# Kernel optimization log

Measured on AMD Instinct MI355X. Metric: run time of the kernel, lower is better.

## Reference

```python
import jax, jax.numpy as jnp
import numpy as np

B, T, V, D, U = 128, 512, 50000, 256, 256


def setup_inputs() -> dict:
    key = jax.random.key(0)
    ks = jax.random.split(key, 16)

    def n(k, shape, s=0.05):
        return jax.random.normal(k, shape, dtype=jnp.float32) * s

    inp = {
        "tokens": jax.random.randint(ks[0], (B, T), 0, V, dtype=jnp.int32),
        "emb": n(ks[1], (V, D)),
    }
    dims = [D, U, U, U]
    i = 2
    for l in range(4):
        inp[f"Wx{l}"] = n(ks[i], (dims[l], 3 * U)); i += 1
        inp[f"Wh{l}"] = n(ks[i], (U, 3 * U)); i += 1
        inp[f"bx{l}"] = jnp.zeros((3 * U,), jnp.float32)
        inp[f"bh{l}"] = jnp.zeros((3 * U,), jnp.float32)
    inp["Wd1"] = n(ks[i], (U, U)); i += 1
    inp["bd1"] = jnp.zeros((U,), jnp.float32)
    inp["Wd2"] = n(ks[i], (U, 1)); i += 1
    inp["bd2"] = jnp.zeros((1,), jnp.float32)
    return inp


def _gru_layer(x_seq, Wx, Wh, bx, bh):
    # x_seq: [T, B, d_in]. Keras GRUCell math with reset_after=True.
    # Precompute all input projections in one big GEMM (efficient form).
    xp = jnp.einsum('tbd,dk->tbk', x_seq, Wx) + bx  # [T, B, 3U]
    h0 = jnp.zeros((x_seq.shape[1], Wh.shape[0]), x_seq.dtype)

    def step(h, xp_t):
        rec = h @ Wh + bh                      # recurrent proj + recurrent bias
        xz, xr, xh = jnp.split(xp_t, 3, axis=-1)
        rz, rr, rh = jnp.split(rec, 3, axis=-1)
        z = jax.nn.sigmoid(xz + rz)            # update gate
        r = jax.nn.sigmoid(xr + rr)            # reset gate
        hh = jnp.tanh(xh + r * rh)             # candidate (reset applied after rec matmul)
        hn = z * h + (1.0 - z) * hh
        return hn, hn

    _, hs = jax.lax.scan(step, h0, xp)
    return hs  # [T, B, U]


def reference(tokens, emb,
              Wx0, Wh0, bx0, bh0,
              Wx1, Wh1, bx1, bh1,
              Wx2, Wh2, bx2, bh2,
              Wx3, Wh3, bx3, bh3,
              Wd1, bd1, Wd2, bd2):
    x = emb[tokens]                    # [B, T, D] embedding lookup
    x = jnp.transpose(x, (1, 0, 2))    # [T, B, D] time-major for scan
    for Wx, Wh, bx, bh in ((Wx0, Wh0, bx0, bh0), (Wx1, Wh1, bx1, bh1),
                           (Wx2, Wh2, bx2, bh2), (Wx3, Wh3, bx3, bh3)):
        x = _gru_layer(x, Wx, Wh, bx, bh)
    out = x[-1]                        # last timestep of top layer: [B, U]
    h = jax.nn.relu(out @ Wd1 + bd1)   # Dense(units) + ReLU (dropout off at inference)
    logit = h @ Wd2 + bd2              # Dense(1)
    return jax.nn.sigmoid(logit)       # [B, 1]
```

## Files before the change

### kernel.cpp

```cpp
#include <hip/hip_runtime.h>
#include <stdint.h>


#define TT 512
#define RX 16
#define RH 64

typedef __bf16 bf16x8 __attribute__((ext_vector_type(8)));
typedef float f32x4 __attribute__((ext_vector_type(4)));
typedef int i32x4 __attribute__((ext_vector_type(4)));

#define FLAGS_BYTES (128*256)
#define XPRING_E ((size_t)RX*768*16)
#define HRING_E  ((size_t)RH*16*256)
#define WS_XP_OFF ((size_t)FLAGS_BYTES)
#define WS_H_OFF  (WS_XP_OFF + (size_t)32*XPRING_E*2)
#define WS_HF_OFF (WS_H_OFF  + (size_t)32*HRING_E*2)

struct Params {
  const int* tokens;
  const float* emb;
  const float* Wx[4];
  const float* Wh[4];
  const float* bx[4];
  const float* bh[4];
  uint8_t* ws;
};

#define SCOPE_AGENT __HIP_MEMORY_SCOPE_AGENT

__device__ __forceinline__ uint32_t* flagp(uint8_t* ws, int kind, int g, int l){
  return (uint32_t*)(ws + ((size_t)(kind*32 + g*4 + l) * 256));
}
__device__ __forceinline__ uint32_t aload(uint32_t* p){
  return __hip_atomic_load(p, __ATOMIC_RELAXED, SCOPE_AGENT);
}
__device__ __forceinline__ void astore(uint32_t* p, uint32_t v){
  __hip_atomic_store(p, v, __ATOMIC_RELAXED, SCOPE_AGENT);
}
__device__ __forceinline__ void st_coh_b64(void* p, unsigned long long v){
  asm volatile("global_store_dwordx2 %0, %1, off sc0 sc1" :: "v"(p), "v"(v) : "memory");
}
__device__ __forceinline__ void st_coh_b128(void* p, i32x4 v){
  asm volatile("global_store_dwordx4 %0, %1, off sc0 sc1" :: "v"(p), "v"(v) : "memory");
}
__device__ __forceinline__ unsigned long long ld_coh_b64(const void* p){
  unsigned long long r;
  asm volatile("global_load_dwordx2 %0, %1, off sc0 sc1" : "=v"(r) : "v"(p));
  return r;
}
__device__ __forceinline__ i32x4 ld_coh_b128(const void* p){
  i32x4 r;
  asm volatile("global_load_dwordx4 %0, %1, off sc0 sc1" : "=v"(r) : "v"(p));
  return r;
}
__device__ __forceinline__ void wait_vm0(){
  asm volatile("s_waitcnt vmcnt(0)" ::: "memory");
}
__device__ __forceinline__ unsigned short f2b(float f){
  __bf16 b = (__bf16)f; unsigned short u; __builtin_memcpy(&u, &b, 2); return u;
}
__device__ __forceinline__ float b2f(unsigned short u){
  __bf16 b; __builtin_memcpy(&b, &u, 2); return (float)b;
}
__device__ __forceinline__ f32x4 up4(unsigned long long q){
  f32x4 r;
  #pragma unroll
  for (int i=0;i<4;++i) r[i] = b2f((unsigned short)(q >> (16*i)));
  return r;
}
__device__ __forceinline__ unsigned long long pk4(f32x4 v){
  unsigned long long q = 0;
  #pragma unroll
  for (int i=0;i<4;++i) q |= ((unsigned long long)f2b(v[i])) << (16*i);
  return q;
}
__device__ __forceinline__ float sigf(float x){ return 1.f/(1.f + __expf(-x)); }
__device__ __forceinline__ float tanh_(float x){ return 2.f/(1.f + __expf(-2.f*x)) - 1.f; }

__global__ __launch_bounds__(512, 2) void gru_pipeline(Params p){
  const int bid = blockIdx.x;
  const int g = bid >> 3;
  const int s = bid & 7;
  const int l = s >> 1;
  const bool isXp = (s & 1) == 0;
  const int tid = threadIdx.x;
  const int w = tid >> 6;
  const int lane = tid & 63;
  const int lg = lane >> 4;
  const int lc = lane & 15;

  __shared__ int dead;
  __shared__ __align__(16) unsigned short h_stage[2][16*256];
  __shared__ __align__(16) unsigned short h_lds[16*256];
  if (tid == 0) dead = 0;
  int budget = 1 << 22;

  if (isXp) {
    const float* W = p.Wx[l];
    bf16x8 wx[6][8];
    #pragma unroll
    for (int nt=0; nt<6; ++nt){
      const int col = w*96 + nt*16 + lc;
      #pragma unroll
      for (int kt=0; kt<8; ++kt){
        const int k0 = kt*32 + lg*8;
        bf16x8 v;
        #pragma unroll
        for (int e=0; e<8; ++e) v[e] = (__bf16)W[(size_t)(k0+e)*768 + col];
        wx[nt][kt] = v;
      }
    }
    float bias[6];
    #pragma unroll
    for (int nt=0; nt<6; ++nt){
      const int col = w*96 + nt*16 + lc;
      bias[nt] = p.bx[l][col] + (col < 512 ? p.bh[l][col] : 0.f);
    }
    uint32_t* prodXp = flagp(p.ws, 0, g, l);
    uint32_t* prodH  = (l>0) ? flagp(p.ws, 1, g, l-1) : nullptr;
    uint32_t* consXp = flagp(p.ws, 2, g, l);
    uint32_t* consH  = (l>0) ? flagp(p.ws, 3, g, l-1) : nullptr;
    __bf16* xr = (__bf16*)(p.ws + WS_XP_OFF) + (size_t)(g*4+l)*XPRING_E;
    const __bf16* hr = (l>0) ? ((const __bf16*)(p.ws + WS_H_OFF) + (size_t)(g*4+(l-1))*HRING_E) : nullptr;
    uint32_t consSeen = 0, prodSeen = 0;
    const int sm = tid >> 5, sc = tid & 31;

    if (l > 0){
      if (tid == 0){
        while (prodSeen < 1u){
          prodSeen = aload(prodH);
          if (prodSeen < 1u){ if(--budget<0){dead=1;break;} __builtin_amdgcn_s_sleep(2); }
        }
      }
      __syncthreads();
      if (!dead){
        i32x4 v = ld_coh_b128(hr + (size_t)sm*256 + sc*8);
        wait_vm0(); __builtin_amdgcn_sched_barrier(0);
        *(i32x4*)&h_stage[0][(sm*256 + sc*8) ^ ((sm&7)<<3)] = v;
      }
    } else {
      const int tok = p.tokens[(size_t)(g*16+sm)*TT];
      const float* er = p.emb + (size_t)tok*256 + sc*8;
      const float4 u0 = *(const float4*)er;
      const float4 u1 = *(const float4*)(er+4);
      bf16x8 v;
      v[0]=(__bf16)u0.x; v[1]=(__bf16)u0.y; v[2]=(__bf16)u0.z; v[3]=(__bf16)u0.w;
      v[4]=(__bf16)u1.x; v[5]=(__bf16)u1.y; v[6]=(__bf16)u1.z; v[7]=(__bf16)u1.w;
      *(bf16x8*)&h_stage[0][(sm*256 + sc*8) ^ ((sm&7)<<3)] = v;
    }

    for (int t=0; t<TT; ++t){
      if (tid == 0){
        if (l > 0){
          const uint32_t need = (uint32_t)((t+2 < TT) ? t+2 : TT);
          while (prodSeen < need){
            prodSeen = aload(prodH);
            if (prodSeen < need){ if(--budget<0){dead=1;break;} __builtin_amdgcn_s_sleep(2); }
          }
        }
        if (t >= RX){
          const uint32_t need2 = (uint32_t)(t - RX + 1);
          while (consSeen < need2){
            consSeen = aload(consXp);
            if (consSeen < need2){ if(--budget<0){dead=1;break;} __builtin_amdgcn_s_sleep(2); }
          }
        }
      }
      __syncthreads();
      if (dead) break;
      if (tid == 0 && t > 0){
        astore(prodXp, (uint32_t)t);
        if (l > 0) astore(consH, (uint32_t)(t+1));
      }

      i32x4 stg;
      const bool haveStg = (l > 0) && (t+1 < TT);
      if (haveStg){
        stg = ld_coh_b128(hr + (size_t)((t+1)&(RH-1))*16*256 + sm*256 + sc*8);
      } else if (l == 0 && t+1 < TT){
        const int tok = p.tokens[(size_t)(g*16+sm)*TT + (t+1)];
        const float* er = p.emb + (size_t)tok*256 + sc*8;
        const float4 u0 = *(const float4*)er;
        const float4 u1 = *(const float4*)(er+4);
        bf16x8 v;
        v[0]=(__bf16)u0.x; v[1]=(__bf16)u0.y; v[2]=(__bf16)u0.z; v[3]=(__bf16)u0.w;
        v[4]=(__bf16)u1.x; v[5]=(__bf16)u1.y; v[6]=(__bf16)u1.z; v[7]=(__bf16)u1.w;
        *(bf16x8*)&h_stage[(t+1)&1][(sm*256 + sc*8) ^ ((sm&7)<<3)] = v;
      }

      const unsigned short* hsrc = h_stage[t&1];
      f32x4 acc[6];
      #pragma unroll
      for (int nt=0; nt<6; ++nt) acc[nt] = (f32x4){bias[nt],bias[nt],bias[nt],bias[nt]};
      #pragma unroll
      for (int kt=0; kt<8; ++kt){
        const bf16x8 a = *(const bf16x8*)&hsrc[(lc*256 + kt*32 + lg*8) ^ ((lc&7)<<3)];
        #pragma unroll
        for (int nt=0; nt<6; ++nt)
          acc[nt] = __builtin_amdgcn_mfma_f32_16x16x32_bf16(a, wx[nt][kt], acc[nt], 0, 0, 0);
      }
      if (haveStg){
        wait_vm0(); __builtin_amdgcn_sched_barrier(0);
        *(i32x4*)&h_stage[(t+1)&1][(sm*256 + sc*8) ^ ((sm&7)<<3)] = stg;
      }
      __bf16* dst = xr + (size_t)(t&(RX-1))*768*16;
      #pragma unroll
      for (int nt=0; nt<6; ++nt){
        const int col = w*96 + nt*16 + lc;
        st_coh_b64(dst + col*16 + lg*4, pk4(acc[nt]));
      }
    }
    wait_vm0();
    __syncthreads();
    if (tid == 0 && !dead){
      astore(prodXp, (uint32_t)TT);
      if (l > 0) astore(consH, (uint32_t)TT);
    }
  } else {
    const float* W = p.Wh[l];
    bf16x8 wh[6][8];
    #pragma unroll
    for (int nt=0; nt<6; ++nt){
      const int col = 256*(nt>>1) + w*32 + 16*(nt&1) + lc;
      #pragma unroll
      for (int kt=0; kt<8; ++kt){
        const int k0 = kt*32 + lg*8;
        bf16x8 v;
        #pragma unroll
        for (int e=0; e<8; ++e) v[e] = (__bf16)W[(size_t)(k0+e)*768 + col];
        wh[nt][kt] = v;
      }
    }
    float bhh[2];
    #pragma unroll
    for (int q=0; q<2; ++q) bhh[q] = p.bh[l][512 + w*32 + 16*q + lc];

    uint32_t* prodXp = flagp(p.ws, 0, g, l);
    uint32_t* prodH  = (l<3) ? flagp(p.ws, 1, g, l) : nullptr;
    uint32_t* consXp = flagp(p.ws, 2, g, l);
    uint32_t* consH  = (l<3) ? flagp(p.ws, 3, g, l) : nullptr;
    const __bf16* xr = (const __bf16*)(p.ws + WS_XP_OFF) + (size_t)(g*4+l)*XPRING_E;
    __bf16* hrw = (l<3) ? ((__bf16*)(p.ws + WS_H_OFF) + (size_t)(g*4+l)*HRING_E) : nullptr;
    float* hf = (float*)(p.ws + WS_HF_OFF);

    for (int i=tid; i<2048; i+=512) ((uint32_t*)h_lds)[i] = 0;
    f32x4 hprev[2] = {(f32x4){0.f,0.f,0.f,0.f},(f32x4){0.f,0.f,0.f,0.f}};
    uint32_t consSeen = 0, prodSeen = 0;

    for (int t=0; t<TT; ++t){
      if (tid == 0){
        while (prodSeen < (uint32_t)(t+1)){
          prodSeen = aload(prodXp);
          if (prodSeen < (uint32_t)(t+1)){ if(--budget<0){dead=1;break;} __builtin_amdgcn_s_sleep(2); }
        }
        if (l < 3 && t > RH){
          while (consSeen < (uint32_t)(t - RH)){
            consSeen = aload(consH);
            if (consSeen < (uint32_t)(t - RH)){ if(--budget<0){dead=1;break;} __builtin_amdgcn_s_sleep(2); }
          }
        }
      }
      __syncthreads();
      if (dead) break;

      const __bf16* xb = xr + (size_t)(t&(RX-1))*768*16;
      unsigned long long xpld[6];
      #pragma unroll
      for (int nt=0; nt<6; ++nt){
        const int col = 256*(nt>>1) + w*32 + 16*(nt&1) + lc;
        xpld[nt] = ld_coh_b64(xb + col*16 + lg*4);
      }
      if (l < 3 && t > 0){
        const i32x4 ev = *(const i32x4*)&h_lds[(lc*256 + w*32 + lg*8) ^ ((lc&7)<<3)];
        st_coh_b128(hrw + (size_t)((t-1)&(RH-1))*16*256 + lc*256 + w*32 + lg*8, ev);
      }
      f32x4 acc[6];
      #pragma unroll
      for (int nt=0; nt<6; ++nt) acc[nt] = (f32x4){0.f,0.f,0.f,0.f};
      #pragma unroll
      for (int kt=0; kt<8; ++kt){
        const bf16x8 a = *(const bf16x8*)&h_lds[(lc*256 + kt*32 + lg*8) ^ ((lc&7)<<3)];
        #pragma unroll
        for (int nt=0; nt<6; ++nt)
          acc[nt] = __builtin_amdgcn_mfma_f32_16x16x32_bf16(a, wh[nt][kt], acc[nt], 0, 0, 0);
      }
      wait_vm0(); __builtin_amdgcn_sched_barrier(0);
      #pragma unroll
      for (int q=0; q<2; ++q){
        const f32x4 xz = up4(xpld[q]);
        const f32x4 xr_ = up4(xpld[2+q]);
        const f32x4 xh = up4(xpld[4+q]);
        #pragma unroll
        for (int e=0; e<4; ++e){
          const float z = sigf(xz[e] + acc[q][e]);
          const float r = sigf(xr_[e] + acc[2+q][e]);
          const float c = tanh_(xh[e] + r*(acc[4+q][e] + bhh[q]));
          hprev[q][e] = z*hprev[q][e] + (1.f - z)*c;
        }
      }
      __syncthreads();
      #pragma unroll
      for (int q=0; q<2; ++q){
        const int j = w*32 + 16*q + lc;
        #pragma unroll
        for (int r2=0; r2<4; ++r2){
          const int m = lg*4 + r2;
          h_lds[(m*256 + j) ^ ((m&7)<<3)] = f2b(hprev[q][r2]);
        }
      }
      if (l == 3 && t == TT-1){
        #pragma unroll
        for (int q=0; q<2; ++q){
          const int j = w*32 + 16*q + lc;
          #pragma unroll
          for (int r2=0; r2<4; ++r2) hf[(size_t)(g*16 + lg*4 + r2)*256 + j] = hprev[q][r2];
        }
      }
      __syncthreads();
      if (tid == 0){
        if (l < 3 && t > 0) astore(prodH, (uint32_t)t);
        astore(consXp, (uint32_t)(t+1));
      }
    }
    if (!dead){
      if (l < 3){
        const i32x4 ev = *(const i32x4*)&h_lds[(lc*256 + w*32 + lg*8) ^ ((lc&7)<<3)];
        st_coh_b128(hrw + (size_t)((TT-1)&(RH-1))*16*256 + lc*256 + w*32 + lg*8, ev);
        wait_vm0();
        __syncthreads();
        if (tid == 0) astore(prodH, (uint32_t)TT);
      }
      if (tid == 0) astore(consXp, (uint32_t)TT);
    }
  }
}

__global__ __launch_bounds__(256) void dense_head(const float* __restrict__ hf,
    const float* __restrict__ Wd1, const float* __restrict__ bd1,
    const float* __restrict__ Wd2, const float* __restrict__ bd2,
    float* __restrict__ out){
  const int m = blockIdx.x;
  const int n = threadIdx.x;
  __shared__ float hs[256];
  __shared__ float red[256];
  hs[n] = hf[(size_t)m*256 + n];
  __syncthreads();
  float acc = bd1[n];
  #pragma unroll 8
  for (int k=0; k<256; ++k) acc = fmaf(hs[k], Wd1[(size_t)k*256 + n], acc);
  const float rl = fmaxf(acc, 0.f);
  red[n] = rl * Wd2[n];
  __syncthreads();
  for (int off=128; off>0; off>>=1){
    if (n < off) red[n] += red[n+off];
    __syncthreads();
  }
  if (n == 0) out[m] = 1.f/(1.f + __expf(-(red[0] + bd2[0])));
}

extern "C" void kernel_launch(void* const* d_in, const int* in_sizes, int n_in,
                              void* d_out, int out_size, void* d_ws, size_t ws_size,
                              hipStream_t stream){
  (void)in_sizes; (void)n_in; (void)out_size; (void)ws_size;
  Params p;
  p.tokens = (const int*)d_in[0];
  p.emb    = (const float*)d_in[1];
  for (int l=0; l<4; ++l){
    p.Wx[l] = (const float*)d_in[2+4*l];
    p.Wh[l] = (const float*)d_in[3+4*l];
    p.bx[l] = (const float*)d_in[4+4*l];
    p.bh[l] = (const float*)d_in[5+4*l];
  }
  p.ws = (uint8_t*)d_ws;
  hipMemsetAsync(d_ws, 0, FLAGS_BYTES, stream);
  gru_pipeline<<<dim3(64), dim3(512), 0, stream>>>(p);
  dense_head<<<dim3(128), dim3(256), 0, stream>>>(
      (const float*)((uint8_t*)d_ws + WS_HF_OFF),
      (const float*)d_in[18], (const float*)d_in[19],
      (const float*)d_in[20], (const float*)d_in[21],
      (float*)d_out);
}
```

Measured before the change: 2.904 ms.

## Batch cross-block flag handshakes every 4 steps and double-buffer recurrent state in LDS

Inter-block producer/consumer flag polling and publishing now happen once per chunk of CH=4 timesteps rather than every step. The recurrent blocks double-buffer the hidden state in shared memory, which removes one barrier per step. They also prefetch the next step's input projection one step ahead, using partial vmcnt waits in place of full drains. This cuts per-step global atomic traffic and barrier latency on the serial recurrence. The cost is coarser pipeline slack, which could delay downstream layers. The hand-counted vmcnt values are fragile and may break ordering.

```diff
diff --git a/kernel.cpp b/kernel.cpp
--- a/kernel.cpp
+++ b/kernel.cpp
@@ -5,6 +5,7 @@
 #define TT 512
 #define RX 16
 #define RH 64
+#define CH 4
 
 typedef __bf16 bf16x8 __attribute__((ext_vector_type(8)));
 typedef float f32x4 __attribute__((ext_vector_type(4)));
@@ -54,9 +55,9 @@
   asm volatile("global_load_dwordx4 %0, %1, off sc0 sc1" : "=v"(r) : "v"(p));
   return r;
 }
-__device__ __forceinline__ void wait_vm0(){
-  asm volatile("s_waitcnt vmcnt(0)" ::: "memory");
-}
+#define WAITVM(N) asm volatile("s_waitcnt vmcnt(" #N ")" ::: "memory")
+#define BARRIER_LGKM() asm volatile("s_waitcnt lgkmcnt(0)\n\ts_barrier" ::: "memory")
+
 __device__ __forceinline__ unsigned short f2b(float f){
   __bf16 b = (__bf16)f; unsigned short u; __builtin_memcpy(&u, &b, 2); return u;
 }
@@ -78,7 +79,7 @@
 __device__ __forceinline__ float sigf(float x){ return 1.f/(1.f + __expf(-x)); }
 __device__ __forceinline__ float tanh_(float x){ return 2.f/(1.f + __expf(-2.f*x)) - 1.f; }
 
-__global__ __launch_bounds__(512, 2) void gru_pipeline(Params p){
+__global__ __launch_bounds__(512) void gru_pipeline(Params p){
   const int bid = blockIdx.x;
   const int g = bid >> 3;
   const int s = bid & 7;
@@ -91,8 +92,7 @@
   const int lc = lane & 15;
 
   __shared__ int dead;
-  __shared__ __align__(16) unsigned short h_stage[2][16*256];
-  __shared__ __align__(16) unsigned short h_lds[16*256];
+  __shared__ __align__(16) unsigned short sbuf[2][16*256];
   if (tid == 0) dead = 0;
   int budget = 1 << 22;
 
@@ -125,6 +125,7 @@
     const __bf16* hr = (l>0) ? ((const __bf16*)(p.ws + WS_H_OFF) + (size_t)(g*4+(l-1))*HRING_E) : nullptr;
     uint32_t consSeen = 0, prodSeen = 0;
     const int sm = tid >> 5, sc = tid & 31;
+    const int sidx = (sm*256 + sc*8) ^ ((sm&7)<<3);
 
     if (l > 0){
       if (tid == 0){
@@ -136,8 +137,8 @@
       __syncthreads();
       if (!dead){
         i32x4 v = ld_coh_b128(hr + (size_t)sm*256 + sc*8);
-        wait_vm0(); __builtin_amdgcn_sched_barrier(0);
-        *(i32x4*)&h_stage[0][(sm*256 + sc*8) ^ ((sm&7)<<3)] = v;
+        WAITVM(0); __builtin_amdgcn_sched_barrier(0);
+        *(i32x4*)&sbuf[0][sidx] = v;
       }
     } else {
       const int tok = p.tokens[(size_t)(g*16+sm)*TT];
@@ -147,49 +148,51 @@
       bf16x8 v;
       v[0]=(__bf16)u0.x; v[1]=(__bf16)u0.y; v[2]=(__bf16)u0.z; v[3]=(__bf16)u0.w;
       v[4]=(__bf16)u1.x; v[5]=(__bf16)u1.y; v[6]=(__bf16)u1.z; v[7]=(__bf16)u1.w;
-      *(bf16x8*)&h_stage[0][(sm*256 + sc*8) ^ ((sm&7)<<3)] = v;
+      *(bf16x8*)&sbuf[0][sidx] = v;
     }
 
     for (int t=0; t<TT; ++t){
-      if (tid == 0){
+      const bool bnd = (t & (CH-1)) == 0;
+      if (bnd){
+        __syncthreads();
+        if (tid == 0){
+          if (l > 0){
+            const uint32_t need = (uint32_t)((t+CH+1 < TT) ? t+CH+1 : TT);
+            while (prodSeen < need){
+              prodSeen = aload(prodH);
+              if (prodSeen < need){ if(--budget<0){dead=1;break;} __builtin_amdgcn_s_sleep(2); }
+            }
+          }
+          if (t + CH - 1 >= RX && !dead){
+            const uint32_t need2 = (uint32_t)(t + CH - RX);
+            while (consSeen < need2){
+              consSeen = aload(consXp);
+              if (consSeen < need2){ if(--budget<0){dead=1;break;} __builtin_amdgcn_s_sleep(2); }
+            }
+          }
+        }
+        __syncthreads();
+        if (dead) break;
+      }
+      i32x4 stg; bf16x8 vnext;
+      const bool havePf = (t+1 < TT);
+      if (havePf){
         if (l > 0){
-          const uint32_t need = (uint32_t)((t+2 < TT) ? t+2 : TT);
-          while (prodSeen < need){
-            prodSeen = aload(prodH);
-            if (prodSeen < need){ if(--budget<0){dead=1;break;} __builtin_amdgcn_s_sleep(2); }
-          }
-        }
-        if (t >= RX){
-          const uint32_t need2 = (uint32_t)(t - RX + 1);
-          while (consSeen < need2){
-            consSeen = aload(consXp);
-            if (consSeen < need2){ if(--budget<0){dead=1;break;} __builtin_amdgcn_s_sleep(2); }
-          }
-        }
-      }
-      __syncthreads();
-      if (dead) break;
-      if (tid == 0 && t > 0){
+          stg = ld_coh_b128(hr + (size_t)((t+1)&(RH-1))*16*256 + sm*256 + sc*8);
+        } else {
+          const int tok = p.tokens[(size_t)(g*16+sm)*TT + (t+1)];
+          const float* er = p.emb + (size_t)tok*256 + sc*8;
+          const float4 u0 = *(const float4*)er;
+          const float4 u1 = *(const float4*)(er+4);
+          vnext[0]=(__bf16)u0.x; vnext[1]=(__bf16)u0.y; vnext[2]=(__bf16)u0.z; vnext[3]=(__bf16)u0.w;
+          vnext[4]=(__bf16)u1.x; vnext[5]=(__bf16)u1.y; vnext[6]=(__bf16)u1.z; vnext[7]=(__bf16)u1.w;
+        }
+      }
+      if (bnd && tid == 0 && t > 0){
         astore(prodXp, (uint32_t)t);
-        if (l > 0) astore(consH, (uint32_t)(t+1));
-      }
-
-      i32x4 stg;
-      const bool haveStg = (l > 0) && (t+1 < TT);
-      if (haveStg){
-        stg = ld_coh_b128(hr + (size_t)((t+1)&(RH-1))*16*256 + sm*256 + sc*8);
-      } else if (l == 0 && t+1 < TT){
-        const int tok = p.tokens[(size_t)(g*16+sm)*TT + (t+1)];
-        const float* er = p.emb + (size_t)tok*256 + sc*8;
-        const float4 u0 = *(const float4*)er;
-        const float4 u1 = *(const float4*)(er+4);
-        bf16x8 v;
-        v[0]=(__bf16)u0.x; v[1]=(__bf16)u0.y; v[2]=(__bf16)u0.z; v[3]=(__bf16)u0.w;
-        v[4]=(__bf16)u1.x; v[5]=(__bf16)u1.y; v[6]=(__bf16)u1.z; v[7]=(__bf16)u1.w;
-        *(bf16x8*)&h_stage[(t+1)&1][(sm*256 + sc*8) ^ ((sm&7)<<3)] = v;
-      }
-
-      const unsigned short* hsrc = h_stage[t&1];
+        if (l > 0) astore(consH, (uint32_t)t);
+      }
+      const unsigned short* hsrc = sbuf[t&1];
       f32x4 acc[6];
       #pragma unroll
       for (int nt=0; nt<6; ++nt) acc[nt] = (f32x4){bias[nt],bias[nt],bias[nt],bias[nt]};
@@ -199,10 +202,6 @@
         #pragma unroll
         for (int nt=0; nt<6; ++nt)
           acc[nt] = __builtin_amdgcn_mfma_f32_16x16x32_bf16(a, wx[nt][kt], acc[nt], 0, 0, 0);
-      }
-      if (haveStg){
-        wait_vm0(); __builtin_amdgcn_sched_barrier(0);
-        *(i32x4*)&h_stage[(t+1)&1][(sm*256 + sc*8) ^ ((sm&7)<<3)] = stg;
       }
       __bf16* dst = xr + (size_t)(t&(RX-1))*768*16;
       #pragma unroll
@@ -210,8 +209,17 @@
         const int col = w*96 + nt*16 + lc;
         st_coh_b64(dst + col*16 + lg*4, pk4(acc[nt]));
       }
-    }
-    wait_vm0();
+      if (havePf){
+        if (l > 0){
+          if (bnd && t > 0) { WAITVM(8); }
+          else             { WAITVM(6); }
+          *(i32x4*)&sbuf[(t+1)&1][sidx] = stg;
+        } else {
+          *(bf16x8*)&sbuf[(t+1)&1][sidx] = vnext;
+        }
+      }
+      BARRIER_LGKM();
+    }
     __syncthreads();
     if (tid == 0 && !dead){
       astore(prodXp, (uint32_t)TT);
@@ -244,53 +252,84 @@
     __bf16* hrw = (l<3) ? ((__bf16*)(p.ws + WS_H_OFF) + (size_t)(g*4+l)*HRING_E) : nullptr;
     float* hf = (float*)(p.ws + WS_HF_OFF);
 
-    for (int i=tid; i<2048; i+=512) ((uint32_t*)h_lds)[i] = 0;
+    for (int i=tid; i<2048; i+=512) ((uint32_t*)sbuf[0])[i] = 0;
     f32x4 hprev[2] = {(f32x4){0.f,0.f,0.f,0.f},(f32x4){0.f,0.f,0.f,0.f}};
     uint32_t consSeen = 0, prodSeen = 0;
 
-    for (int t=0; t<TT; ++t){
-      if (tid == 0){
-        while (prodSeen < (uint32_t)(t+1)){
-          prodSeen = aload(prodXp);
-          if (prodSeen < (uint32_t)(t+1)){ if(--budget<0){dead=1;break;} __builtin_amdgcn_s_sleep(2); }
-        }
-        if (l < 3 && t > RH){
-          while (consSeen < (uint32_t)(t - RH)){
-            consSeen = aload(consH);
-            if (consSeen < (uint32_t)(t - RH)){ if(--budget<0){dead=1;break;} __builtin_amdgcn_s_sleep(2); }
-          }
-        }
-      }
-      __syncthreads();
-      if (dead) break;
-
-      const __bf16* xb = xr + (size_t)(t&(RX-1))*768*16;
-      unsigned long long xpld[6];
+    if (tid == 0){
+      while (prodSeen < 1u){
+        prodSeen = aload(prodXp);
+        if (prodSeen < 1u){ if(--budget<0){dead=1;break;} __builtin_amdgcn_s_sleep(2); }
+      }
+    }
+    __syncthreads();
+    unsigned long long xpc[6], xpn[6];
+    if (!dead){
       #pragma unroll
       for (int nt=0; nt<6; ++nt){
         const int col = 256*(nt>>1) + w*32 + 16*(nt&1) + lc;
-        xpld[nt] = ld_coh_b64(xb + col*16 + lg*4);
-      }
+        xpc[nt] = ld_coh_b64(xr + col*16 + lg*4);
+      }
+    }
+
+    for (int t=0; t<TT; ++t){
+      const bool bnd = (t & (CH-1)) == 0;
+      if (bnd){
+        __syncthreads();
+        if (tid == 0){
+          const uint32_t need = (uint32_t)((t+CH+1 < TT) ? t+CH+1 : TT);
+          while (prodSeen < need){
+            prodSeen = aload(prodXp);
+            if (prodSeen < need){ if(--budget<0){dead=1;break;} __builtin_amdgcn_s_sleep(2); }
+          }
+          if (l < 3 && t + CH - 1 > RH && !dead){
+            const uint32_t need2 = (uint32_t)(t + CH - 1 - RH);
+            while (consSeen < need2){
+              consSeen = aload(consH);
+              if (consSeen < need2){ if(--budget<0){dead=1;break;} __builtin_amdgcn_s_sleep(2); }
+            }
+          }
+        }
+        __syncthreads();
+        if (dead) break;
+        if (tid == 0 && t > 0){
+          astore(consXp, (uint32_t)t);
+          if (l < 3) astore(prodH, (uint32_t)(t-1));
+        }
+      }
+      const unsigned short* hsrc = sbuf[t&1];
       if (l < 3 && t > 0){
-        const i32x4 ev = *(const i32x4*)&h_lds[(lc*256 + w*32 + lg*8) ^ ((lc&7)<<3)];
+        const i32x4 ev = *(const i32x4*)&hsrc[(lc*256 + w*32 + lg*8) ^ ((lc&7)<<3)];
         st_coh_b128(hrw + (size_t)((t-1)&(RH-1))*16*256 + lc*256 + w*32 + lg*8, ev);
       }
+      if (t+1 < TT){
+        const __bf16* xb = xr + (size_t)((t+1)&(RX-1))*768*16;
+        #pragma unroll
+        for (int nt=0; nt<6; ++nt){
+          const int col = 256*(nt>>1) + w*32 + 16*(nt&1) + lc;
+          xpn[nt] = ld_coh_b64(xb + col*16 + lg*4);
+        }
+      }
       f32x4 acc[6];
       #pragma unroll
       for (int nt=0; nt<6; ++nt) acc[nt] = (f32x4){0.f,0.f,0.f,0.f};
       #pragma unroll
       for (int kt=0; kt<8; ++kt){
-        const bf16x8 a = *(const bf16x8*)&h_lds[(lc*256 + kt*32 + lg*8) ^ ((lc&7)<<3)];
+        const bf16x8 a = *(const bf16x8*)&hsrc[(lc*256 + kt*32 + lg*8) ^ ((lc&7)<<3)];
         #pragma unroll
         for (int nt=0; nt<6; ++nt)
           acc[nt] = __builtin_amdgcn_mfma_f32_16x16x32_bf16(a, wh[nt][kt], acc[nt], 0, 0, 0);
       }
-      wait_vm0(); __builtin_amdgcn_sched_barrier(0);
+      if (!bnd){
+        if (t+1 < TT){ if (l < 3) { WAITVM(7); } else { WAITVM(6); } }
+        else         { if (l < 3) { WAITVM(1); } else { WAITVM(0); } }
+      }
+      __builtin_amdgcn_sched_barrier(0);
       #pragma unroll
       for (int q=0; q<2; ++q){
-        const f32x4 xz = up4(xpld[q]);
-        const f32x4 xr_ = up4(xpld[2+q]);
-        const f32x4 xh = up4(xpld[4+q]);
+        const f32x4 xz = up4(xpc[q]);
+        const f32x4 xr_ = up4(xpc[2+q]);
+        const f32x4 xh = up4(xpc[4+q]);
         #pragma unroll
         for (int e=0; e<4; ++e){
           const float z = sigf(xz[e] + acc[q][e]);
@@ -299,14 +338,14 @@
           hprev[q][e] = z*hprev[q][e] + (1.f - z)*c;
         }
       }
-      __syncthreads();
+      unsigned short* hdst = sbuf[(t+1)&1];
       #pragma unroll
       for (int q=0; q<2; ++q){
         const int j = w*32 + 16*q + lc;
         #pragma unroll
         for (int r2=0; r2<4; ++r2){
           const int m = lg*4 + r2;
-          h_lds[(m*256 + j) ^ ((m&7)<<3)] = f2b(hprev[q][r2]);
+          hdst[(m*256 + j) ^ ((m&7)<<3)] = f2b(hprev[q][r2]);
         }
       }
       if (l == 3 && t == TT-1){
@@ -317,21 +356,20 @@
           for (int r2=0; r2<4; ++r2) hf[(size_t)(g*16 + lg*4 + r2)*256 + j] = hprev[q][r2];
         }
       }
+      BARRIER_LGKM();
+      #pragma unroll
+      for (int nt=0; nt<6; ++nt) xpc[nt] = xpn[nt];
+    }
+    if (!dead){
+      if (l < 3){
+        const i32x4 ev = *(const i32x4*)&sbuf[0][(lc*256 + w*32 + lg*8) ^ ((lc&7)<<3)];
+        st_coh_b128(hrw + (size_t)((TT-1)&(RH-1))*16*256 + lc*256 + w*32 + lg*8, ev);
+      }
       __syncthreads();
       if (tid == 0){
-        if (l < 3 && t > 0) astore(prodH, (uint32_t)t);
-        astore(consXp, (uint32_t)(t+1));
-      }
-    }
-    if (!dead){
-      if (l < 3){
-        const i32x4 ev = *(const i32x4*)&h_lds[(lc*256 + w*32 + lg*8) ^ ((lc&7)<<3)];
-        st_coh_b128(hrw + (size_t)((TT-1)&(RH-1))*16*256 + lc*256 + w*32 + lg*8, ev);
-        wait_vm0();
-        __syncthreads();
-        if (tid == 0) astore(prodH, (uint32_t)TT);
-      }
-      if (tid == 0) astore(consXp, (uint32_t)TT);
+        if (l < 3) astore(prodH, (uint32_t)TT);
+        astore(consXp, (uint32_t)TT);
+      }
     }
   }
 }
```

After: 3.373 ms. 1.16x slower.
